# Performance work log

Hardware: AMD Instinct MI355X
Metric: run time of the kernel (lower is better)

## Reference

```python
import jax, jax.numpy as jnp
import numpy as np

B, S, T = 128, 512, 256


def setup_inputs() -> dict:
    key = jax.random.key(0)
    k1, k2, k3, k4 = jax.random.split(key, 4)
    emissions = jax.random.normal(k1, (B, S, T), dtype=jnp.float32)
    mask = jnp.ones((B, S), dtype=bool)
    transitions = jax.random.normal(k2, (T, T), dtype=jnp.float32)
    start_transitions = jax.random.normal(k3, (T,), dtype=jnp.float32)
    end_transitions = jax.random.normal(k4, (T,), dtype=jnp.float32)
    return {
        "emissions": emissions,
        "mask": mask,
        "transitions": transitions,
        "start_transitions": start_transitions,
        "end_transitions": end_transitions,
    }


def reference(emissions, mask, transitions, start_transitions, end_transitions):
    """Batched Viterbi decode. Returns (paths [B,S] int32, best_scores [B] f32).

    Faithful to CRFLayer._viterbi_decode: score_0 = start + em_0; at each step
    next[i,j] = score[i] + trans[i,j] + em_t[j], take max/argmax over i; add
    end_transitions at the end; backtrack via backpointers. Masked (padded)
    steps carry score through unchanged with identity backpointers, so padded
    tail positions replicate the last valid tag (mask is all-ones here, so
    output equals the original's full-length paths).
    """
    Bn, Sn, Tn = emissions.shape
    ident = jnp.arange(Tn, dtype=jnp.int32)
    score0 = start_transitions[None, :] + emissions[:, 0]  # [B,T]

    em_ts = jnp.swapaxes(emissions, 0, 1)[1:]  # [S-1,B,T]
    m_ts = jnp.swapaxes(mask, 0, 1)[1:]        # [S-1,B]

    def step(score, inp):
        em_t, m_t = inp
        # nxt[b,i,j] = score[b,i] + trans[i,j] + em_t[b,j]
        nxt = score[:, :, None] + transitions[None, :, :] + em_t[:, None, :]
        best = jnp.max(nxt, axis=1)                    # [B,T]
        idx = jnp.argmax(nxt, axis=1).astype(jnp.int32)  # [B,T] best prev tag
        m = m_t[:, None]
        new_score = jnp.where(m, best, score)
        bp = jnp.where(m, idx, ident[None, :])
        return new_score, bp

    final_score, history = jax.lax.scan(step, score0, (em_ts, m_ts))  # history [S-1,B,T]
    final_score = final_score + end_transitions[None, :]
    best_scores = jnp.max(final_score, axis=1)                         # [B]
    last_tag = jnp.argmax(final_score, axis=1).astype(jnp.int32)       # [B]

    def back(tag, hist_t):
        prev = jnp.take_along_axis(hist_t, tag[:, None], axis=1)[:, 0]
        return prev, tag  # carry prev tag, emit current tag

    first_tag, tags_rest = jax.lax.scan(back, last_tag, history, reverse=True)
    # tags_rest[t] = tag at position t+1; first_tag = tag at position 0
    paths = jnp.concatenate([first_tag[:, None], jnp.swapaxes(tags_rest, 0, 1)], axis=1)
    return paths, best_scores
```

## Files before the change

### kernel.cpp

```cpp
#include <hip/hip_runtime.h>

#define Bn 128
#define Sn 512
#define Tn 256

typedef float v4f __attribute__((ext_vector_type(4)));

template <int CTRL>
__device__ __forceinline__ float dpp_fmax(float v) {
  int x = __builtin_amdgcn_mov_dpp(__float_as_int(v), CTRL, 0xF, 0xF, true);
  return fmaxf(v, __int_as_float(x));
}
__device__ __forceinline__ float row_fmax16(float v) {
  v = dpp_fmax<0x128>(v);
  v = dpp_fmax<0x124>(v);
  v = dpp_fmax<0x122>(v);
  v = dpp_fmax<0x121>(v);
  return v;
}
__device__ __forceinline__ float wave_fmax64(float v) {
  v = row_fmax16(v);
  int x = __builtin_amdgcn_ds_swizzle(__float_as_int(v), 0x401F);
  v = fmaxf(v, __int_as_float(x));
  v = fmaxf(v, __shfl_xor(v, 32));
  return v;
}
__device__ __forceinline__ float readlane_f(float v, int l) {
  return __int_as_float(__builtin_amdgcn_readlane(__float_as_int(v), l));
}

__global__ __launch_bounds__(256) void transpose_kernel(
    const float* __restrict__ tr, float* __restrict__ trT) {
  int idx = blockIdx.x * 256 + threadIdx.x;
  int i = idx >> 8;
  int j = idx & 255;
  trT[j * Tn + i] = tr[i * Tn + j];
}

__global__ __launch_bounds__(1024, 4) void viterbi_fwd(
    const float* __restrict__ em,
    const float* __restrict__ trans,
    const float* __restrict__ start,
    float* __restrict__ scores)
{
  const int b    = blockIdx.x;
  const int tid  = threadIdx.x;
  const int lane = tid & 63;
  const int w    = tid >> 6;
  const int ip   = lane >> 2;
  const int jq   = lane & 3;
  const int jbase = w * 16 + jq * 4;
  const int i0    = ip * 16;
  const int b2 = (lane >> 2) & 1;
  const int b3 = (lane >> 3) & 1;
  const int myc = jbase + b2 * 2 + b3;
  const bool writer = (lane & 48) == 0;

  __shared__ float sbuf[2][Tn];

  float4 tr[16];
#pragma unroll
  for (int k = 0; k < 16; ++k)
    tr[k] = *reinterpret_cast<const float4*>(trans + (i0 + k) * Tn + jbase);

  const float* emb = em + (size_t)b * Sn * Tn;
  float* scb = scores + (size_t)b * Sn * Tn;

  if (tid < 64) {
    int j4 = tid * 4;
    float4 st = *reinterpret_cast<const float4*>(start + j4);
    float4 e0 = *reinterpret_cast<const float4*>(emb + j4);
    float4 s0 = make_float4(st.x + e0.x, st.y + e0.y, st.z + e0.z, st.w + e0.w);
    *reinterpret_cast<float4*>(&sbuf[0][j4]) = s0;
    *reinterpret_cast<float4*>(scb + j4) = s0;
  }

  const float* em_pre = emb + 2 * Tn + myc;
  float*       sc_w   = scb + Tn + myc;
  float e_cur = 0.0f;
  if (writer) e_cur = emb[Tn + myc];
  __syncthreads();

  int cur = 0;
  for (int t = 1; t < Sn; ++t) {
    const float* sp = &sbuf[cur][i0];
    float4 a0 = *reinterpret_cast<const float4*>(sp);
    float4 a1 = *reinterpret_cast<const float4*>(sp + 4);
    float4 a2 = *reinterpret_cast<const float4*>(sp + 8);
    float4 a3 = *reinterpret_cast<const float4*>(sp + 12);

    float e_nxt = 0.0f;
    if (writer) {
      const float* p = (t + 1 < Sn) ? em_pre : em_pre - Tn;
      e_nxt = *p;
    }

    float se[16] = {a0.x,a0.y,a0.z,a0.w, a1.x,a1.y,a1.z,a1.w,
                    a2.x,a2.y,a2.z,a2.w, a3.x,a3.y,a3.z,a3.w};

    float m0 = fmaxf(fmaxf(se[0]+tr[0].x, se[1]+tr[1].x), se[2]+tr[2].x);
    float m1 = fmaxf(fmaxf(se[0]+tr[0].y, se[1]+tr[1].y), se[2]+tr[2].y);
    float m2 = fmaxf(fmaxf(se[0]+tr[0].z, se[1]+tr[1].z), se[2]+tr[2].z);
    float m3 = fmaxf(fmaxf(se[0]+tr[0].w, se[1]+tr[1].w), se[2]+tr[2].w);
#pragma unroll
    for (int k = 3; k < 15; k += 2) {
      m0 = fmaxf(fmaxf(m0, se[k]+tr[k].x), se[k+1]+tr[k+1].x);
      m1 = fmaxf(fmaxf(m1, se[k]+tr[k].y), se[k+1]+tr[k+1].y);
      m2 = fmaxf(fmaxf(m2, se[k]+tr[k].z), se[k+1]+tr[k+1].z);
      m3 = fmaxf(fmaxf(m3, se[k]+tr[k].w), se[k+1]+tr[k+1].w);
    }
    m0 = fmaxf(m0, se[15]+tr[15].x);
    m1 = fmaxf(m1, se[15]+tr[15].y);
    m2 = fmaxf(m2, se[15]+tr[15].z);
    m3 = fmaxf(m3, se[15]+tr[15].w);

    float sA = b2 ? m0 : m2;
    float rA = __shfl_xor(sA, 4);
    float sB = b2 ? m1 : m3;
    float rB = __shfl_xor(sB, 4);
    float p0 = fmaxf(b2 ? m2 : m0, rA);
    float p1 = fmaxf(b2 ? m3 : m1, rB);
    float sC = b3 ? p0 : p1;
    float rC = __shfl_xor(sC, 8);
    float q  = fmaxf(b3 ? p1 : p0, rC);
    q = fmaxf(q, __shfl_xor(q, 16));
    q = fmaxf(q, __shfl_xor(q, 32));

    if (writer) {
      float ns = q + e_cur;
      sbuf[cur ^ 1][myc] = ns;
      *sc_w = ns;
    }
    e_cur = e_nxt;
    em_pre += Tn;
    sc_w   += Tn;
    cur ^= 1;
    __syncthreads();
  }
}

__global__ __launch_bounds__(64, 1) void viterbi_bwd(
    const float* __restrict__ em,
    const float* __restrict__ trT,
    const float* __restrict__ endt,
    const float* __restrict__ scores,
    float* __restrict__ out)
{
  const int b = blockIdx.x;
  const int lane = threadIdx.x;
  const float* scb = scores + (size_t)b * Sn * Tn;
  const float* emb = em + (size_t)b * Sn * Tn;
  const int base = lane * 4;
  const int BIG = 1 << 30;

  __shared__ unsigned char pbuf[Sn];

  float warm = 0.0f;
  for (int off = base; off < Tn * Tn; off += 256) {
    float4 wv = *reinterpret_cast<const float4*>(trT + off);
    warm += wv.x + wv.y + wv.z + wv.w;
  }
  warm *= 0.0f;

  float4 s = *reinterpret_cast<const float4*>(scb + (size_t)(Sn - 1) * Tn + base);
  float4 e = *reinterpret_cast<const float4*>(endt + base);
  float d0 = (s.x + e.x) + warm;
  float d1 = (s.y + e.y) + warm;
  float d2 = (s.z + e.z) + warm;
  float d3 = (s.w + e.w) + warm;
  float bv = fmaxf(fmaxf(fmaxf(d0, d1), d2), d3);
  bv = wave_fmax64(bv);
  int li = BIG;
  if (d3 == bv) li = base + 3;
  if (d2 == bv) li = base + 2;
  if (d1 == bv) li = base + 1;
  if (d0 == bv) li = base;
  unsigned long long mk = __ballot(li != BIG);
  int tag = __shfl(li, (int)__ffsll((long long)mk) - 1);
  if (lane == 0) {
    out[Bn * Sn + b] = bv;
    pbuf[Sn - 1] = (unsigned char)tag;
  }

  #define LD_SR(kk, v0, v1, v2, v3) {                          \
    const float* _p = scb + (size_t)(kk) * Tn + lane;          \
    v0 = __builtin_nontemporal_load(_p);                       \
    v1 = __builtin_nontemporal_load(_p + 64);                  \
    v2 = __builtin_nontemporal_load(_p + 128);                 \
    v3 = __builtin_nontemporal_load(_p + 192); }

  float sP0, sP1, sP2, sP3;
  float sv0, sv1, sv2, sv3;
  float sB0, sB1, sB2, sB3;
  LD_SR(Sn - 1, sP0, sP1, sP2, sP3);
  LD_SR(Sn - 2, sv0, sv1, sv2, sv3);
  LD_SR(Sn - 3, sB0, sB1, sB2, sB3);
  v4f e4  = __builtin_nontemporal_load(
      reinterpret_cast<const v4f*>(emb + (size_t)(Sn - 1) * Tn + base));
  v4f e4B = __builtin_nontemporal_load(
      reinterpret_cast<const v4f*>(emb + (size_t)(Sn - 2) * Tn + base));

  for (int k = Sn - 2; k >= 0; --k) {
    const float* tp = trT + (size_t)tag * Tn + lane;
    float tv0 = tp[0], tv1 = tp[64], tv2 = tp[128], tv3 = tp[192];
    __builtin_amdgcn_sched_barrier(0);

    int kp = (k >= 2) ? k - 2 : 0;
    int ke = (k >= 1) ? k - 1 : 0;
    float sN0, sN1, sN2, sN3;
    LD_SR(kp, sN0, sN1, sN2, sN3);
    v4f e4N = __builtin_nontemporal_load(
        reinterpret_cast<const v4f*>(emb + (size_t)ke * Tn + base));
    __builtin_amdgcn_sched_barrier(0);

    int cs = tag >> 6;
    float sPs = (cs == 0) ? sP0 : (cs == 1) ? sP1 : (cs == 2) ? sP2 : sP3;
    float dmax = readlane_f(sPs, tag & 63);
    int comp = tag & 3;
    float es = (comp == 0) ? e4.x : (comp == 1) ? e4.y
             : (comp == 2) ? e4.z : e4.w;
    float ev = readlane_f(es, tag >> 2);

    float c0 = (sv0 + tv0) + ev;
    float c1 = (sv1 + tv1) + ev;
    float c2 = (sv2 + tv2) + ev;
    float c3 = (sv3 + tv3) + ev;
    unsigned long long m0 = __ballot(c0 == dmax);
    unsigned long long m1 = __ballot(c1 == dmax);
    unsigned long long m2 = __ballot(c2 == dmax);
    unsigned long long m3 = __ballot(c3 == dmax);
    int f0 = (int)__ffsll((long long)m0);
    int f1 = (int)__ffsll((long long)m1);
    int f2 = (int)__ffsll((long long)m2);
    int f3 = (int)__ffsll((long long)m3);
    tag = f0 ? (f0 - 1)
        : f1 ? (63 + f1)
        : f2 ? (127 + f2)
             : (191 + f3);
    if (lane == 0) pbuf[k] = (unsigned char)tag;

    sP0 = sv0; sP1 = sv1; sP2 = sv2; sP3 = sv3;
    sv0 = sB0; sv1 = sB1; sv2 = sB2; sv3 = sB3;
    sB0 = sN0; sB1 = sN1; sB2 = sN2; sB3 = sN3;
    e4 = e4B; e4B = e4N;
  }
  #undef LD_SR

  __syncthreads();
  for (int s2 = lane; s2 < Sn; s2 += 64)
    out[(size_t)b * Sn + s2] = (float)pbuf[s2];
}

extern "C" void kernel_launch(void* const* d_in, const int* in_sizes, int n_in,
                              void* d_out, int out_size, void* d_ws, size_t ws_size,
                              hipStream_t stream) {
  const float* em    = (const float*)d_in[0];
  const float* trans = (const float*)d_in[2];
  const float* start = (const float*)d_in[3];
  const float* endt  = (const float*)d_in[4];
  float* out = (float*)d_out;

  float* scores = (float*)d_ws;
  float* trT = (float*)((char*)d_ws + (size_t)Bn * Sn * Tn * 4);

  transpose_kernel<<<Tn * Tn / 256, 256, 0, stream>>>(trans, trT);
  viterbi_fwd<<<Bn, 1024, 0, stream>>>(em, trans, start, scores);
  viterbi_bwd<<<Bn, 64, 0, stream>>>(em, trT, endt, scores, out);
}
```

Before: 720.2 us.

## Remap forward lanes for DPP row reductions and vectorize backward loads

The forward kernel reassigns lanes so that the 16 i-partitions sit within a single DPP row. The cross-lane max then uses row_fmax16 on four values instead of a chain of shfl_xor exchanges through LDS, and every lane now loads its emission value, not only the writers. The backward kernel switches the score and transition reads from four strided scalar loads per lane to one float4 load per lane. Its tag selection is rewritten to find the lowest index across the interleaved layout. This aims to shorten the per-step latency of the serial forward and backward chains, at the cost of four DPP reductions per step instead of a merged butterfly.

```diff
diff --git a/kernel.cpp b/kernel.cpp
--- a/kernel.cpp
+++ b/kernel.cpp
@@ -47,21 +47,19 @@
   const int tid  = threadIdx.x;
   const int lane = tid & 63;
   const int w    = tid >> 6;
-  const int ip   = lane >> 2;
-  const int jq   = lane & 3;
+  const int ip   = lane & 15;
+  const int jq   = lane >> 4;
   const int jbase = w * 16 + jq * 4;
   const int i0    = ip * 16;
-  const int b2 = (lane >> 2) & 1;
-  const int b3 = (lane >> 3) & 1;
-  const int myc = jbase + b2 * 2 + b3;
-  const bool writer = (lane & 48) == 0;
+  const bool writer = (ip < 4);
+  const int mycol = w * 16 + jq * 4 + (ip & 3);
 
   __shared__ float sbuf[2][Tn];
 
   float4 tr[16];
 #pragma unroll
   for (int k = 0; k < 16; ++k)
-    tr[k] = *reinterpret_cast<const float4*>(trans + (i0 + k) * Tn + jbase);
+    tr[k] = *reinterpret_cast<const float4*>(trans + (size_t)(i0 + k) * Tn + jbase);
 
   const float* emb = em + (size_t)b * Sn * Tn;
   float* scb = scores + (size_t)b * Sn * Tn;
@@ -75,10 +73,9 @@
     *reinterpret_cast<float4*>(scb + j4) = s0;
   }
 
-  const float* em_pre = emb + 2 * Tn + myc;
-  float*       sc_w   = scb + Tn + myc;
-  float e_cur = 0.0f;
-  if (writer) e_cur = emb[Tn + myc];
+  const float* em_pre = emb + 2 * Tn + mycol;
+  float*       sc_w   = scb + Tn + mycol;
+  float e_cur = emb[Tn + mycol];
   __syncthreads();
 
   int cur = 0;
@@ -89,11 +86,8 @@
     float4 a2 = *reinterpret_cast<const float4*>(sp + 8);
     float4 a3 = *reinterpret_cast<const float4*>(sp + 12);
 
-    float e_nxt = 0.0f;
-    if (writer) {
-      const float* p = (t + 1 < Sn) ? em_pre : em_pre - Tn;
-      e_nxt = *p;
-    }
+    const float* pe = (t + 1 < Sn) ? em_pre : em_pre - Tn;
+    float e_nxt = *pe;
 
     float se[16] = {a0.x,a0.y,a0.z,a0.w, a1.x,a1.y,a1.z,a1.w,
                     a2.x,a2.y,a2.z,a2.w, a3.x,a3.y,a3.z,a3.w};
@@ -114,21 +108,15 @@
     m2 = fmaxf(m2, se[15]+tr[15].z);
     m3 = fmaxf(m3, se[15]+tr[15].w);
 
-    float sA = b2 ? m0 : m2;
-    float rA = __shfl_xor(sA, 4);
-    float sB = b2 ? m1 : m3;
-    float rB = __shfl_xor(sB, 4);
-    float p0 = fmaxf(b2 ? m2 : m0, rA);
-    float p1 = fmaxf(b2 ? m3 : m1, rB);
-    float sC = b3 ? p0 : p1;
-    float rC = __shfl_xor(sC, 8);
-    float q  = fmaxf(b3 ? p1 : p0, rC);
-    q = fmaxf(q, __shfl_xor(q, 16));
-    q = fmaxf(q, __shfl_xor(q, 32));
+    m0 = row_fmax16(m0);
+    m1 = row_fmax16(m1);
+    m2 = row_fmax16(m2);
+    m3 = row_fmax16(m3);
 
     if (writer) {
-      float ns = q + e_cur;
-      sbuf[cur ^ 1][myc] = ns;
+      float mv = (ip == 0) ? m0 : (ip == 1) ? m1 : (ip == 2) ? m2 : m3;
+      float ns = mv + e_cur;
+      sbuf[cur ^ 1][mycol] = ns;
       *sc_w = ns;
     }
     e_cur = e_nxt;
@@ -182,49 +170,36 @@
     pbuf[Sn - 1] = (unsigned char)tag;
   }
 
-  #define LD_SR(kk, v0, v1, v2, v3) {                          \
-    const float* _p = scb + (size_t)(kk) * Tn + lane;          \
-    v0 = __builtin_nontemporal_load(_p);                       \
-    v1 = __builtin_nontemporal_load(_p + 64);                  \
-    v2 = __builtin_nontemporal_load(_p + 128);                 \
-    v3 = __builtin_nontemporal_load(_p + 192); }
-
-  float sP0, sP1, sP2, sP3;
-  float sv0, sv1, sv2, sv3;
-  float sB0, sB1, sB2, sB3;
-  LD_SR(Sn - 1, sP0, sP1, sP2, sP3);
-  LD_SR(Sn - 2, sv0, sv1, sv2, sv3);
-  LD_SR(Sn - 3, sB0, sB1, sB2, sB3);
-  v4f e4  = __builtin_nontemporal_load(
-      reinterpret_cast<const v4f*>(emb + (size_t)(Sn - 1) * Tn + base));
-  v4f e4B = __builtin_nontemporal_load(
-      reinterpret_cast<const v4f*>(emb + (size_t)(Sn - 2) * Tn + base));
+  #define LD_V4(ptr) __builtin_nontemporal_load(reinterpret_cast<const v4f*>(ptr))
+
+  v4f sP = LD_V4(scb + (size_t)(Sn - 1) * Tn + base);
+  v4f sv = LD_V4(scb + (size_t)(Sn - 2) * Tn + base);
+  v4f sB = LD_V4(scb + (size_t)(Sn - 3) * Tn + base);
+  v4f e4  = LD_V4(emb + (size_t)(Sn - 1) * Tn + base);
+  v4f e4B = LD_V4(emb + (size_t)(Sn - 2) * Tn + base);
 
   for (int k = Sn - 2; k >= 0; --k) {
-    const float* tp = trT + (size_t)tag * Tn + lane;
-    float tv0 = tp[0], tv1 = tp[64], tv2 = tp[128], tv3 = tp[192];
+    float4 tv = *reinterpret_cast<const float4*>(trT + (size_t)tag * Tn + base);
     __builtin_amdgcn_sched_barrier(0);
 
     int kp = (k >= 2) ? k - 2 : 0;
     int ke = (k >= 1) ? k - 1 : 0;
-    float sN0, sN1, sN2, sN3;
-    LD_SR(kp, sN0, sN1, sN2, sN3);
-    v4f e4N = __builtin_nontemporal_load(
-        reinterpret_cast<const v4f*>(emb + (size_t)ke * Tn + base));
+    v4f sN  = LD_V4(scb + (size_t)kp * Tn + base);
+    v4f e4N = LD_V4(emb + (size_t)ke * Tn + base);
     __builtin_amdgcn_sched_barrier(0);
 
-    int cs = tag >> 6;
-    float sPs = (cs == 0) ? sP0 : (cs == 1) ? sP1 : (cs == 2) ? sP2 : sP3;
-    float dmax = readlane_f(sPs, tag & 63);
     int comp = tag & 3;
+    float sPs = (comp == 0) ? sP.x : (comp == 1) ? sP.y
+              : (comp == 2) ? sP.z : sP.w;
+    float dmax = readlane_f(sPs, tag >> 2);
     float es = (comp == 0) ? e4.x : (comp == 1) ? e4.y
              : (comp == 2) ? e4.z : e4.w;
     float ev = readlane_f(es, tag >> 2);
 
-    float c0 = (sv0 + tv0) + ev;
-    float c1 = (sv1 + tv1) + ev;
-    float c2 = (sv2 + tv2) + ev;
-    float c3 = (sv3 + tv3) + ev;
+    float c0 = (sv.x + tv.x) + ev;
+    float c1 = (sv.y + tv.y) + ev;
+    float c2 = (sv.z + tv.z) + ev;
+    float c3 = (sv.w + tv.w) + ev;
     unsigned long long m0 = __ballot(c0 == dmax);
     unsigned long long m1 = __ballot(c1 == dmax);
     unsigned long long m2 = __ballot(c2 == dmax);
@@ -233,18 +208,19 @@
     int f1 = (int)__ffsll((long long)m1);
     int f2 = (int)__ffsll((long long)m2);
     int f3 = (int)__ffsll((long long)m3);
-    tag = f0 ? (f0 - 1)
-        : f1 ? (63 + f1)
-        : f2 ? (127 + f2)
-             : (191 + f3);
+    int i0 = f0 ? ((f0 - 1) * 4 + 0) : BIG;
+    int i1 = f1 ? ((f1 - 1) * 4 + 1) : BIG;
+    int i2 = f2 ? ((f2 - 1) * 4 + 2) : BIG;
+    int i3 = f3 ? ((f3 - 1) * 4 + 3) : BIG;
+    int ta = (i0 < i1) ? i0 : i1;
+    int tb = (i2 < i3) ? i2 : i3;
+    tag = (ta < tb) ? ta : tb;
     if (lane == 0) pbuf[k] = (unsigned char)tag;
 
-    sP0 = sv0; sP1 = sv1; sP2 = sv2; sP3 = sv3;
-    sv0 = sB0; sv1 = sB1; sv2 = sB2; sv3 = sB3;
-    sB0 = sN0; sB1 = sN1; sB2 = sN2; sB3 = sN3;
+    sP = sv; sv = sB; sB = sN;
     e4 = e4B; e4B = e4N;
   }
-  #undef LD_SR
+  #undef LD_V4
 
   __syncthreads();
   for (int s2 = lane; s2 < Sn; s2 += 64)
```

New measurement: 828.3 us. 15.0% more time.

## Halve forward block size with two columns per thread; restructure backtrack loop

Applied to the files above, without the earlier changes.

The forward kernel now runs with 512 threads per block, and each thread handles two 16-column groups of the transition matrix instead of one. This doubles the register-resident transition tiles and the reduction work per thread, with the aim of cutting barrier cost and wave count per step. The backward kernel is rewritten to load contiguous float4 score rows in a rotating 4-stage unrolled ring, fetch the emission scalar directly, and keep the tag uniform via readfirstlane, with the goal of shortening the serial dependency chain per step. The higher register use in the forward kernel may cause spills.

```diff
diff --git a/kernel.cpp b/kernel.cpp
--- a/kernel.cpp
+++ b/kernel.cpp
@@ -37,7 +37,7 @@
   trT[j * Tn + i] = tr[i * Tn + j];
 }
 
-__global__ __launch_bounds__(1024, 4) void viterbi_fwd(
+__global__ __launch_bounds__(512, 2) void viterbi_fwd(
     const float* __restrict__ em,
     const float* __restrict__ trans,
     const float* __restrict__ start,
@@ -49,19 +49,23 @@
   const int w    = tid >> 6;
   const int ip   = lane >> 2;
   const int jq   = lane & 3;
-  const int jbase = w * 16 + jq * 4;
-  const int i0    = ip * 16;
+  const int jbA  = w * 32 + jq * 4;
+  const int jbB  = jbA + 16;
+  const int i0   = ip * 16;
   const int b2 = (lane >> 2) & 1;
   const int b3 = (lane >> 3) & 1;
-  const int myc = jbase + b2 * 2 + b3;
+  const int mycA = jbA + b2 * 2 + b3;
+  const int mycB = mycA + 16;
   const bool writer = (lane & 48) == 0;
 
   __shared__ float sbuf[2][Tn];
 
-  float4 tr[16];
+  float4 tr_a[16], tr_b[16];
 #pragma unroll
-  for (int k = 0; k < 16; ++k)
-    tr[k] = *reinterpret_cast<const float4*>(trans + (i0 + k) * Tn + jbase);
+  for (int k = 0; k < 16; ++k) {
+    tr_a[k] = *reinterpret_cast<const float4*>(trans + (size_t)(i0 + k) * Tn + jbA);
+    tr_b[k] = *reinterpret_cast<const float4*>(trans + (size_t)(i0 + k) * Tn + jbB);
+  }
 
   const float* emb = em + (size_t)b * Sn * Tn;
   float* scb = scores + (size_t)b * Sn * Tn;
@@ -75,10 +79,15 @@
     *reinterpret_cast<float4*>(scb + j4) = s0;
   }
 
-  const float* em_pre = emb + 2 * Tn + myc;
-  float*       sc_w   = scb + Tn + myc;
-  float e_cur = 0.0f;
-  if (writer) e_cur = emb[Tn + myc];
+  const float* em_preA = emb + 2 * Tn + mycA;
+  const float* em_preB = emb + 2 * Tn + mycB;
+  float* sc_wA = scb + Tn + mycA;
+  float* sc_wB = scb + Tn + mycB;
+  float e_curA = 0.0f, e_curB = 0.0f;
+  if (writer) {
+    e_curA = emb[Tn + mycA];
+    e_curB = emb[Tn + mycB];
+  }
   __syncthreads();
 
   int cur = 0;
@@ -89,30 +98,44 @@
     float4 a2 = *reinterpret_cast<const float4*>(sp + 8);
     float4 a3 = *reinterpret_cast<const float4*>(sp + 12);
 
-    float e_nxt = 0.0f;
+    float e_nxtA = 0.0f, e_nxtB = 0.0f;
     if (writer) {
-      const float* p = (t + 1 < Sn) ? em_pre : em_pre - Tn;
-      e_nxt = *p;
+      const float* pA = (t + 1 < Sn) ? em_preA : em_preA - Tn;
+      const float* pB = (t + 1 < Sn) ? em_preB : em_preB - Tn;
+      e_nxtA = *pA;
+      e_nxtB = *pB;
     }
 
     float se[16] = {a0.x,a0.y,a0.z,a0.w, a1.x,a1.y,a1.z,a1.w,
                     a2.x,a2.y,a2.z,a2.w, a3.x,a3.y,a3.z,a3.w};
 
-    float m0 = fmaxf(fmaxf(se[0]+tr[0].x, se[1]+tr[1].x), se[2]+tr[2].x);
-    float m1 = fmaxf(fmaxf(se[0]+tr[0].y, se[1]+tr[1].y), se[2]+tr[2].y);
-    float m2 = fmaxf(fmaxf(se[0]+tr[0].z, se[1]+tr[1].z), se[2]+tr[2].z);
-    float m3 = fmaxf(fmaxf(se[0]+tr[0].w, se[1]+tr[1].w), se[2]+tr[2].w);
+    float m0 = fmaxf(fmaxf(se[0]+tr_a[0].x, se[1]+tr_a[1].x), se[2]+tr_a[2].x);
+    float m1 = fmaxf(fmaxf(se[0]+tr_a[0].y, se[1]+tr_a[1].y), se[2]+tr_a[2].y);
+    float m2 = fmaxf(fmaxf(se[0]+tr_a[0].z, se[1]+tr_a[1].z), se[2]+tr_a[2].z);
+    float m3 = fmaxf(fmaxf(se[0]+tr_a[0].w, se[1]+tr_a[1].w), se[2]+tr_a[2].w);
+    float n0 = fmaxf(fmaxf(se[0]+tr_b[0].x, se[1]+tr_b[1].x), se[2]+tr_b[2].x);
+    float n1 = fmaxf(fmaxf(se[0]+tr_b[0].y, se[1]+tr_b[1].y), se[2]+tr_b[2].y);
+    float n2 = fmaxf(fmaxf(se[0]+tr_b[0].z, se[1]+tr_b[1].z), se[2]+tr_b[2].z);
+    float n3 = fmaxf(fmaxf(se[0]+tr_b[0].w, se[1]+tr_b[1].w), se[2]+tr_b[2].w);
 #pragma unroll
     for (int k = 3; k < 15; k += 2) {
-      m0 = fmaxf(fmaxf(m0, se[k]+tr[k].x), se[k+1]+tr[k+1].x);
-      m1 = fmaxf(fmaxf(m1, se[k]+tr[k].y), se[k+1]+tr[k+1].y);
-      m2 = fmaxf(fmaxf(m2, se[k]+tr[k].z), se[k+1]+tr[k+1].z);
-      m3 = fmaxf(fmaxf(m3, se[k]+tr[k].w), se[k+1]+tr[k+1].w);
+      m0 = fmaxf(fmaxf(m0, se[k]+tr_a[k].x), se[k+1]+tr_a[k+1].x);
+      m1 = fmaxf(fmaxf(m1, se[k]+tr_a[k].y), se[k+1]+tr_a[k+1].y);
+      m2 = fmaxf(fmaxf(m2, se[k]+tr_a[k].z), se[k+1]+tr_a[k+1].z);
+      m3 = fmaxf(fmaxf(m3, se[k]+tr_a[k].w), se[k+1]+tr_a[k+1].w);
+      n0 = fmaxf(fmaxf(n0, se[k]+tr_b[k].x), se[k+1]+tr_b[k+1].x);
+      n1 = fmaxf(fmaxf(n1, se[k]+tr_b[k].y), se[k+1]+tr_b[k+1].y);
+      n2 = fmaxf(fmaxf(n2, se[k]+tr_b[k].z), se[k+1]+tr_b[k+1].z);
+      n3 = fmaxf(fmaxf(n3, se[k]+tr_b[k].w), se[k+1]+tr_b[k+1].w);
     }
-    m0 = fmaxf(m0, se[15]+tr[15].x);
-    m1 = fmaxf(m1, se[15]+tr[15].y);
-    m2 = fmaxf(m2, se[15]+tr[15].z);
-    m3 = fmaxf(m3, se[15]+tr[15].w);
+    m0 = fmaxf(m0, se[15]+tr_a[15].x);
+    m1 = fmaxf(m1, se[15]+tr_a[15].y);
+    m2 = fmaxf(m2, se[15]+tr_a[15].z);
+    m3 = fmaxf(m3, se[15]+tr_a[15].w);
+    n0 = fmaxf(n0, se[15]+tr_b[15].x);
+    n1 = fmaxf(n1, se[15]+tr_b[15].y);
+    n2 = fmaxf(n2, se[15]+tr_b[15].z);
+    n3 = fmaxf(n3, se[15]+tr_b[15].w);
 
     float sA = b2 ? m0 : m2;
     float rA = __shfl_xor(sA, 4);
@@ -122,18 +145,35 @@
     float p1 = fmaxf(b2 ? m3 : m1, rB);
     float sC = b3 ? p0 : p1;
     float rC = __shfl_xor(sC, 8);
-    float q  = fmaxf(b3 ? p1 : p0, rC);
-    q = fmaxf(q, __shfl_xor(q, 16));
-    q = fmaxf(q, __shfl_xor(q, 32));
+    float qA = fmaxf(b3 ? p1 : p0, rC);
+    qA = fmaxf(qA, __shfl_xor(qA, 16));
+    qA = fmaxf(qA, __shfl_xor(qA, 32));
+    float sD = b2 ? n0 : n2;
+    float rD = __shfl_xor(sD, 4);
+    float sE = b2 ? n1 : n3;
+    float rE = __shfl_xor(sE, 4);
+    float u0 = fmaxf(b2 ? n2 : n0, rD);
+    float u1 = fmaxf(b2 ? n3 : n1, rE);
+    float sF = b3 ? u0 : u1;
+    float rF = __shfl_xor(sF, 8);
+    float qB = fmaxf(b3 ? u1 : u0, rF);
+    qB = fmaxf(qB, __shfl_xor(qB, 16));
+    qB = fmaxf(qB, __shfl_xor(qB, 32));
 
     if (writer) {
-      float ns = q + e_cur;
-      sbuf[cur ^ 1][myc] = ns;
-      *sc_w = ns;
+      float nsA = qA + e_curA;
+      float nsB = qB + e_curB;
+      sbuf[cur ^ 1][mycA] = nsA;
+      sbuf[cur ^ 1][mycB] = nsB;
+      *sc_wA = nsA;
+      *sc_wB = nsB;
     }
-    e_cur = e_nxt;
-    em_pre += Tn;
-    sc_w   += Tn;
+    e_curA = e_nxtA;
+    e_curB = e_nxtB;
+    em_preA += Tn;
+    em_preB += Tn;
+    sc_wA += Tn;
+    sc_wB += Tn;
     cur ^= 1;
     __syncthreads();
   }
@@ -181,70 +221,68 @@
     out[Bn * Sn + b] = bv;
     pbuf[Sn - 1] = (unsigned char)tag;
   }
-
-  #define LD_SR(kk, v0, v1, v2, v3) {                          \
-    const float* _p = scb + (size_t)(kk) * Tn + lane;          \
-    v0 = __builtin_nontemporal_load(_p);                       \
-    v1 = __builtin_nontemporal_load(_p + 64);                  \
-    v2 = __builtin_nontemporal_load(_p + 128);                 \
-    v3 = __builtin_nontemporal_load(_p + 192); }
-
-  float sP0, sP1, sP2, sP3;
-  float sv0, sv1, sv2, sv3;
-  float sB0, sB1, sB2, sB3;
-  LD_SR(Sn - 1, sP0, sP1, sP2, sP3);
-  LD_SR(Sn - 2, sv0, sv1, sv2, sv3);
-  LD_SR(Sn - 3, sB0, sB1, sB2, sB3);
-  v4f e4  = __builtin_nontemporal_load(
-      reinterpret_cast<const v4f*>(emb + (size_t)(Sn - 1) * Tn + base));
-  v4f e4B = __builtin_nontemporal_load(
-      reinterpret_cast<const v4f*>(emb + (size_t)(Sn - 2) * Tn + base));
-
-  for (int k = Sn - 2; k >= 0; --k) {
-    const float* tp = trT + (size_t)tag * Tn + lane;
-    float tv0 = tp[0], tv1 = tp[64], tv2 = tp[128], tv3 = tp[192];
-    __builtin_amdgcn_sched_barrier(0);
-
-    int kp = (k >= 2) ? k - 2 : 0;
-    int ke = (k >= 1) ? k - 1 : 0;
-    float sN0, sN1, sN2, sN3;
-    LD_SR(kp, sN0, sN1, sN2, sN3);
-    v4f e4N = __builtin_nontemporal_load(
-        reinterpret_cast<const v4f*>(emb + (size_t)ke * Tn + base));
-    __builtin_amdgcn_sched_barrier(0);
-
-    int cs = tag >> 6;
-    float sPs = (cs == 0) ? sP0 : (cs == 1) ? sP1 : (cs == 2) ? sP2 : sP3;
-    float dmax = readlane_f(sPs, tag & 63);
-    int comp = tag & 3;
-    float es = (comp == 0) ? e4.x : (comp == 1) ? e4.y
-             : (comp == 2) ? e4.z : e4.w;
-    float ev = readlane_f(es, tag >> 2);
-
-    float c0 = (sv0 + tv0) + ev;
-    float c1 = (sv1 + tv1) + ev;
-    float c2 = (sv2 + tv2) + ev;
-    float c3 = (sv3 + tv3) + ev;
-    unsigned long long m0 = __ballot(c0 == dmax);
-    unsigned long long m1 = __ballot(c1 == dmax);
-    unsigned long long m2 = __ballot(c2 == dmax);
-    unsigned long long m3 = __ballot(c3 == dmax);
-    int f0 = (int)__ffsll((long long)m0);
-    int f1 = (int)__ffsll((long long)m1);
-    int f2 = (int)__ffsll((long long)m2);
-    int f3 = (int)__ffsll((long long)m3);
-    tag = f0 ? (f0 - 1)
-        : f1 ? (63 + f1)
-        : f2 ? (127 + f2)
-             : (191 + f3);
-    if (lane == 0) pbuf[k] = (unsigned char)tag;
-
-    sP0 = sv0; sP1 = sv1; sP2 = sv2; sP3 = sv3;
-    sv0 = sB0; sv1 = sB1; sv2 = sB2; sv3 = sB3;
-    sB0 = sN0; sB1 = sN1; sB2 = sN2; sB3 = sN3;
-    e4 = e4B; e4B = e4N;
-  }
-  #undef LD_SR
+  tag = __builtin_amdgcn_readfirstlane(tag);
+
+  #define LD_V4(ptr) __builtin_nontemporal_load(reinterpret_cast<const v4f*>(ptr))
+
+  v4f S0, S1, S2, S3;
+  S3 = LD_V4(scb + (size_t)(Sn - 1) * Tn + base);
+  S2 = LD_V4(scb + (size_t)(Sn - 2) * Tn + base);
+  S1 = LD_V4(scb + (size_t)(Sn - 3) * Tn + base);
+
+  #define BWD_STEP(kk_, SP_, SC_, SN_) {                                     \
+    const int k_ = (kk_);                                                    \
+                           \
+    float4 tv = *reinterpret_cast<const float4*>(trT + (size_t)tag * Tn + base); \
+    __builtin_amdgcn_sched_barrier(0);                                       \
+                   \
+    float ev = emb[(size_t)(k_ + 1) * Tn + tag];                             \
+    __builtin_amdgcn_sched_barrier(0);                                       \
+             \
+    int kp_ = (k_ >= 2) ? k_ - 2 : 0;                                        \
+    SN_ = LD_V4(scb + (size_t)kp_ * Tn + base);                              \
+    __builtin_amdgcn_sched_barrier(0);                                       \
+                                             \
+    int comp_ = tag & 3;                                                     \
+    float sPs_ = (comp_ == 0) ? SP_.x : (comp_ == 1) ? SP_.y                 \
+               : (comp_ == 2) ? SP_.z : SP_.w;                               \
+    float dmax_ = readlane_f(sPs_, tag >> 2);                                \
+                       \
+    float c0_ = (SC_.x + tv.x) + ev;                                         \
+    float c1_ = (SC_.y + tv.y) + ev;                                         \
+    float c2_ = (SC_.z + tv.z) + ev;                                         \
+    float c3_ = (SC_.w + tv.w) + ev;                                         \
+    unsigned long long m0_ = __ballot(c0_ == dmax_);                         \
+    unsigned long long m1_ = __ballot(c1_ == dmax_);                         \
+    unsigned long long m2_ = __ballot(c2_ == dmax_);                         \
+    unsigned long long m3_ = __ballot(c3_ == dmax_);                         \
+    int f0_ = (int)__ffsll((long long)m0_);                                  \
+    int f1_ = (int)__ffsll((long long)m1_);                                  \
+    int f2_ = (int)__ffsll((long long)m2_);                                  \
+    int f3_ = (int)__ffsll((long long)m3_);                                  \
+    int i0_ = f0_ ? ((f0_ - 1) * 4 + 0) : BIG;                               \
+    int i1_ = f1_ ? ((f1_ - 1) * 4 + 1) : BIG;                               \
+    int i2_ = f2_ ? ((f2_ - 1) * 4 + 2) : BIG;                               \
+    int i3_ = f3_ ? ((f3_ - 1) * 4 + 3) : BIG;                               \
+    int ta_ = (i0_ < i1_) ? i0_ : i1_;                                       \
+    int tb_ = (i2_ < i3_) ? i2_ : i3_;                                       \
+    tag = (ta_ < tb_) ? ta_ : tb_;                                           \
+    tag = __builtin_amdgcn_readfirstlane(tag);                               \
+    if (lane == 0) pbuf[k_] = (unsigned char)tag;                            \
+  }
+
+  for (int kk = Sn - 2; kk >= 3; kk -= 4) {
+    BWD_STEP(kk,     S3, S2, S0);
+    BWD_STEP(kk - 1, S2, S1, S3);
+    BWD_STEP(kk - 2, S1, S0, S2);
+    BWD_STEP(kk - 3, S0, S3, S1);
+  }
+  BWD_STEP(2, S3, S2, S0);
+  BWD_STEP(1, S2, S1, S3);
+  BWD_STEP(0, S1, S0, S2);
+
+  #undef BWD_STEP
+  #undef LD_V4
 
   __syncthreads();
   for (int s2 = lane; s2 < Sn; s2 += 64)
@@ -264,6 +302,6 @@
   float* trT = (float*)((char*)d_ws + (size_t)Bn * Sn * Tn * 4);
 
   transpose_kernel<<<Tn * Tn / 256, 256, 0, stream>>>(trans, trT);
-  viterbi_fwd<<<Bn, 1024, 0, stream>>>(em, trans, start, scores);
+  viterbi_fwd<<<Bn, 512, 0, stream>>>(em, trans, start, scores);
   viterbi_bwd<<<Bn, 64, 0, stream>>>(em, trT, endt, scores, out);
 }
```

Measured after the change: 864.5 us. +20.0%, slower.
